# Kernel optimization log

Hardware: AMD Instinct MI355X
Metric: run time of the kernel (lower is better)

## Reference

```python
import jax, jax.numpy as jnp
import numpy as np

N_HEADS = 4
N_HIDDEN = 64  # out_features (concat=False)
MASK_FILL = -9e15
ADJ_THRESH = 0.05


def setup_inputs() -> dict:
    key = jax.random.key(0)
    k1, k2, k3, k4 = jax.random.split(key, 4)
    B, S, N, F = 32, 20, 128, 64
    h = jax.random.normal(k1, (B, S, N, F), dtype=jnp.float32)
    adj_mat = jax.random.uniform(k2, (B, S, N, N), dtype=jnp.float32)
    W = jax.random.normal(k3, (F, N_HEADS * N_HIDDEN), dtype=jnp.float32) * (1.0 / np.sqrt(F))
    a = jax.random.normal(k4, (N_HEADS, 2 * N_HIDDEN, 1), dtype=jnp.float32) * 0.1
    return {"h": h, "adj_mat": adj_mat, "W": W, "a": a}


def reference(h, adj_mat, W, a):
    B, S, N, _ = h.shape
    # Linear projection (no bias); dropout is a no-op (training=False)
    ht = jnp.einsum('bsnf,fo->bsno', h, W)
    # (B, S, H, N, D)
    ht = ht.reshape(B, S, N, N_HEADS, N_HIDDEN).transpose(0, 1, 3, 2, 4)
    a_src = a[:, :N_HIDDEN, 0]   # (H, D)
    a_tgt = a[:, N_HIDDEN:, 0]   # (H, D)
    src = jnp.einsum('bshnd,hd->bshn', ht, a_src)  # (B,S,H,N)
    tgt = jnp.einsum('bshnd,hd->bshn', ht, a_tgt)
    # additive sigmoid score: e_ij = sigmoid(src_i + tgt_j)
    e = jax.nn.sigmoid(src[..., :, None] + tgt[..., None, :])  # (B,S,H,N,N)
    mask = (adj_mat < ADJ_THRESH)[:, :, None, :, :]  # broadcast over heads
    e = jnp.where(mask, MASK_FILL, e)
    attn = jax.nn.softmax(e, axis=-1)
    h_prime = jnp.einsum('bshij,bshjd->bshid', attn, ht)
    # concat=False -> mean over heads
    return h_prime.mean(axis=2)  # (B,S,N,D)
```

## Files before the change

kernel.cpp:

```cpp
#include <hip/hip_runtime.h>
#include <hip/hip_bf16.h>

#define ADJ_TH 0.05f

typedef __bf16 bf16x8 __attribute__((ext_vector_type(8)));
typedef __bf16 bf16x4 __attribute__((ext_vector_type(4)));
typedef float  f32x4  __attribute__((ext_vector_type(4)));

__global__ __launch_bounds__(256)
void prep_kernel(const float* __restrict__ W, const float* __restrict__ a,
                 __bf16* __restrict__ Wt, __bf16* __restrict__ WAt) {
    const int t = threadIdx.x, blk = blockIdx.x;
    if (blk < 64) {
        int id = blk * 256 + t;
        int o = id >> 6, k = id & 63;
        Wt[o * 64 + k] = (__bf16)W[k * 256 + o];
    } else if (blk < 72) {
        int n = blk - 64, hh = n >> 1, st = n & 1;
        int f = t >> 2, p = t & 3;
        const float* wp = W + f * 256 + hh * 64 + p * 16;
        const float* ap = a + hh * 128 + st * 64 + p * 16;
        float s = 0.f;
        #pragma unroll
        for (int d = 0; d < 16; ++d) s += wp[d] * ap[d];
        s += __shfl_xor(s, 1);
        s += __shfl_xor(s, 2);
        if (p == 0) WAt[n * 64 + f] = (__bf16)s;
    } else {
        WAt[512 + t] = (__bf16)0.f;
        WAt[768 + t] = (__bf16)0.f;
    }
}

__device__ __forceinline__ int sw_idx(int o, int i) {
    return o * 128 + ((((i >> 3) ^ o) & 15) << 3) + (i & 7);
}

__global__ __launch_bounds__(256, 3)
void gat_main_kernel(const float* __restrict__ hg, const float* __restrict__ adj,
                     const __bf16* __restrict__ Wt, const __bf16* __restrict__ WAt,
                     float* __restrict__ out)
{
    const int bs  = blockIdx.x;
    const int tid = threadIdx.x;
    const int w   = tid >> 6;
    const int l   = tid & 63;
    const int l15 = l & 15;
    const int l4  = l >> 4;

    __shared__ __bf16   ht_t[128 * 128];
    __shared__ float    src_sh[4][128];
    __shared__ float    tgt_sh[4][128];
    __shared__ unsigned mask_sh[512];

    const float* hb = hg  + (size_t)bs * 8192;
    const float* ab = adj + (size_t)bs * 16384;

    bf16x8 af[2][2];
    #pragma unroll
    for (int m2 = 0; m2 < 2; ++m2) {
        int row = 16 * (2 * w + m2) + l15;
        #pragma unroll
        for (int ks = 0; ks < 2; ++ks) {
            const float4* p4 = reinterpret_cast<const float4*>(hb + row * 64 + 8 * l4 + 32 * ks);
            float4 lo = p4[0], hi = p4[1];
            bf16x8 v;
            v[0]=(__bf16)lo.x; v[1]=(__bf16)lo.y; v[2]=(__bf16)lo.z; v[3]=(__bf16)lo.w;
            v[4]=(__bf16)hi.x; v[5]=(__bf16)hi.y; v[6]=(__bf16)hi.z; v[7]=(__bf16)hi.w;
            af[m2][ks] = v;
        }
    }

    {
        bf16x8 wa0 = *reinterpret_cast<const bf16x8*>(WAt + l15 * 64 + 8 * l4);
        bf16x8 wa1 = *reinterpret_cast<const bf16x8*>(WAt + l15 * 64 + 8 * l4 + 32);
        #pragma unroll
        for (int m2 = 0; m2 < 2; ++m2) {
            f32x4 acc = {0.f,0.f,0.f,0.f};
            acc = __builtin_amdgcn_mfma_f32_16x16x32_bf16(af[m2][0], wa0, acc, 0,0,0);
            acc = __builtin_amdgcn_mfma_f32_16x16x32_bf16(af[m2][1], wa1, acc, 0,0,0);
            if (l15 < 8) {
                int hh = l15 >> 1;
                float* dst = (l15 & 1) ? tgt_sh[hh] : src_sh[hh];
                int i0 = 16 * (2 * w + m2) + 4 * l4;
                #pragma unroll
                for (int r = 0; r < 4; ++r) dst[i0 + r] = acc[r];
            }
        }
    }

    auto gemm1 = [&](int p) {
        #pragma unroll
        for (int nt = 0; nt < 8; ++nt) {
            int oloc = 16 * nt + l15;
            const __bf16* wp = Wt + (size_t)(128 * p + oloc) * 64 + 8 * l4;
            bf16x8 b0 = *reinterpret_cast<const bf16x8*>(wp);
            bf16x8 b1 = *reinterpret_cast<const bf16x8*>(wp + 32);
            #pragma unroll
            for (int m2 = 0; m2 < 2; ++m2) {
                f32x4 acc = {0.f,0.f,0.f,0.f};
                acc = __builtin_amdgcn_mfma_f32_16x16x32_bf16(af[m2][0], b0, acc, 0,0,0);
                acc = __builtin_amdgcn_mfma_f32_16x16x32_bf16(af[m2][1], b1, acc, 0,0,0);
                int i0 = 16 * (2 * w + m2) + 4 * l4;
                bf16x4 st;
                st[0]=(__bf16)acc[0]; st[1]=(__bf16)acc[1];
                st[2]=(__bf16)acc[2]; st[3]=(__bf16)acc[3];
                *reinterpret_cast<bf16x4*>(&ht_t[sw_idx(oloc, i0)]) = st;
            }
        }
    };

    gemm1(0);

    #pragma unroll 4
    for (int rd = 0; rd < 16; ++rd) {
        float4 f = *reinterpret_cast<const float4*>(ab + rd * 1024 + w * 256 + 4 * l);
        unsigned long long b0 = __ballot(f.x < ADJ_TH);
        unsigned long long b1 = __ballot(f.y < ADJ_TH);
        unsigned long long b2 = __ballot(f.z < ADJ_TH);
        unsigned long long b3 = __ballot(f.w < ADJ_TH);
        if (l < 2) {
            int row = 8 * rd + 2 * w + l;
            uint4 v;
            v.x = (unsigned)(b0 >> (32 * l));
            v.y = (unsigned)(b1 >> (32 * l));
            v.z = (unsigned)(b2 >> (32 * l));
            v.w = (unsigned)(b3 >> (32 * l));
            *reinterpret_cast<uint4*>(&mask_sh[row * 4]) = v;
        }
    }

    f32x4 acc2[2][4];
    #pragma unroll
    for (int m2 = 0; m2 < 2; ++m2)
        #pragma unroll
        for (int nt = 0; nt < 4; ++nt) { f32x4 z = {0.f,0.f,0.f,0.f}; acc2[m2][nt] = z; }

    auto phase2 = [&](int p) {
        #pragma unroll 1
        for (int hp = 0; hp < 2; ++hp) {
            int hh = 2 * p + hp;
            float tg[4][8];
            #pragma unroll
            for (int ks = 0; ks < 4; ++ks) {
                const float4* tp = reinterpret_cast<const float4*>(&tgt_sh[hh][8 * l4 + 32 * ks]);
                float4 t0 = tp[0], t1 = tp[1];
                tg[ks][0]=t0.x; tg[ks][1]=t0.y; tg[ks][2]=t0.z; tg[ks][3]=t0.w;
                tg[ks][4]=t1.x; tg[ks][5]=t1.y; tg[ks][6]=t1.z; tg[ks][7]=t1.w;
            }

            bf16x8 pa[2][4];
            #pragma unroll
            for (int m2 = 0; m2 < 2; ++m2) {
                int irow = 16 * (2 * w + m2) + l15;
                float si = src_sh[hh][irow];
                uint4 mm = *reinterpret_cast<const uint4*>(&mask_sh[irow * 4]);
                unsigned mw[4] = {mm.x, mm.y, mm.z, mm.w};
                float pf[4][8];
                float dloc = 0.f;
                #pragma unroll
                for (int ks = 0; ks < 4; ++ks) {
                    #pragma unroll
                    for (int e = 0; e < 8; ++e) {
                        float x  = si + tg[ks][e];
                        float sg = __builtin_amdgcn_rcpf(1.0f + __expf(-x));
                        float pe = __expf(sg);
                        float pv = ((mw[e & 3] >> (8 * ks + 2 * l4 + (e >> 2))) & 1u) ? 0.f : pe;
                        pf[ks][e] = pv;
                        dloc += pv;
                    }
                }
                dloc += __shfl_xor(dloc, 16);
                dloc += __shfl_xor(dloc, 32);
                float scale = 0.25f * __builtin_amdgcn_rcpf(fmaxf(dloc, 1e-20f));
                #pragma unroll
                for (int ks = 0; ks < 4; ++ks) {
                    bf16x8 v;
                    #pragma unroll
                    for (int e = 0; e < 8; ++e) v[e] = (__bf16)(pf[ks][e] * scale);
                    pa[m2][ks] = v;
                }
            }

            #pragma unroll
            for (int nt = 0; nt < 4; ++nt)
                #pragma unroll
                for (int ks = 0; ks < 4; ++ks) {
                    bf16x8 b = *reinterpret_cast<const bf16x8*>(
                        &ht_t[sw_idx(64 * hp + 16 * nt + l15, 8 * l4 + 32 * ks)]);
                    acc2[0][nt] = __builtin_amdgcn_mfma_f32_16x16x32_bf16(pa[0][ks], b, acc2[0][nt], 0,0,0);
                    acc2[1][nt] = __builtin_amdgcn_mfma_f32_16x16x32_bf16(pa[1][ks], b, acc2[1][nt], 0,0,0);
                }
        }
    };

    __syncthreads();
    phase2(0);
    __syncthreads();
    gemm1(1);
    __syncthreads();
    phase2(1);

    float* ob = out + (size_t)bs * 8192;
    #pragma unroll
    for (int m2 = 0; m2 < 2; ++m2)
        #pragma unroll
        for (int nt = 0; nt < 4; ++nt)
            #pragma unroll
            for (int r = 0; r < 4; ++r)
                ob[(32 * w + 16 * m2 + 4 * l4 + r) * 64 + 16 * nt + l15] = acc2[m2][nt][r];
}

extern "C" void kernel_launch(void* const* d_in, const int* in_sizes, int n_in,
                              void* d_out, int out_size, void* d_ws, size_t ws_size,
                              hipStream_t stream) {
    const float* h   = (const float*)d_in[0];
    const float* adj = (const float*)d_in[1];
    const float* W   = (const float*)d_in[2];
    const float* a   = (const float*)d_in[3];
    float* out = (float*)d_out;

    __bf16* Wt  = (__bf16*)d_ws;
    __bf16* WAt = (__bf16*)((char*)d_ws + 32768);

    prep_kernel<<<73, 256, 0, stream>>>(W, a, Wt, WAt);
    gat_main_kernel<<<640, 256, 0, stream>>>(h, adj, Wt, WAt, out);
}
```

Baseline: 138.3 us.

## Use 8 waves per block with one 16-row tile per wave

The main kernel now launches 512 threads per block instead of 256. Each of the 8 waves owns a single 16-row slab instead of two, so the per-wave projection, softmax and attention-matmul work is halved and registers per wave go down. The launch bounds move to (512, 6) to allow more resident waves and more latency hiding on the exp-heavy softmax. In exchange, each wave now reloads the shared weight and ht_t tiles for only half the rows, which doubles LDS read traffic per output row, and __syncthreads now spans more waves.

```diff
diff --git a/kernel.cpp b/kernel.cpp
--- a/kernel.cpp
+++ b/kernel.cpp
@@ -36,7 +36,7 @@
     return o * 128 + ((((i >> 3) ^ o) & 15) << 3) + (i & 7);
 }
 
-__global__ __launch_bounds__(256, 3)
+__global__ __launch_bounds__(512, 6)
 void gat_main_kernel(const float* __restrict__ hg, const float* __restrict__ adj,
                      const __bf16* __restrict__ Wt, const __bf16* __restrict__ WAt,
                      float* __restrict__ out)
@@ -56,10 +56,9 @@
     const float* hb = hg  + (size_t)bs * 8192;
     const float* ab = adj + (size_t)bs * 16384;
 
-    bf16x8 af[2][2];
-    #pragma unroll
-    for (int m2 = 0; m2 < 2; ++m2) {
-        int row = 16 * (2 * w + m2) + l15;
+    bf16x8 af[2];
+    {
+        int row = 16 * w + l15;
         #pragma unroll
         for (int ks = 0; ks < 2; ++ks) {
             const float4* p4 = reinterpret_cast<const float4*>(hb + row * 64 + 8 * l4 + 32 * ks);
@@ -67,25 +66,22 @@
             bf16x8 v;
             v[0]=(__bf16)lo.x; v[1]=(__bf16)lo.y; v[2]=(__bf16)lo.z; v[3]=(__bf16)lo.w;
             v[4]=(__bf16)hi.x; v[5]=(__bf16)hi.y; v[6]=(__bf16)hi.z; v[7]=(__bf16)hi.w;
-            af[m2][ks] = v;
+            af[ks] = v;
         }
     }
 
     {
         bf16x8 wa0 = *reinterpret_cast<const bf16x8*>(WAt + l15 * 64 + 8 * l4);
         bf16x8 wa1 = *reinterpret_cast<const bf16x8*>(WAt + l15 * 64 + 8 * l4 + 32);
-        #pragma unroll
-        for (int m2 = 0; m2 < 2; ++m2) {
-            f32x4 acc = {0.f,0.f,0.f,0.f};
-            acc = __builtin_amdgcn_mfma_f32_16x16x32_bf16(af[m2][0], wa0, acc, 0,0,0);
-            acc = __builtin_amdgcn_mfma_f32_16x16x32_bf16(af[m2][1], wa1, acc, 0,0,0);
-            if (l15 < 8) {
-                int hh = l15 >> 1;
-                float* dst = (l15 & 1) ? tgt_sh[hh] : src_sh[hh];
-                int i0 = 16 * (2 * w + m2) + 4 * l4;
-                #pragma unroll
-                for (int r = 0; r < 4; ++r) dst[i0 + r] = acc[r];
-            }
+        f32x4 acc = {0.f,0.f,0.f,0.f};
+        acc = __builtin_amdgcn_mfma_f32_16x16x32_bf16(af[0], wa0, acc, 0,0,0);
+        acc = __builtin_amdgcn_mfma_f32_16x16x32_bf16(af[1], wa1, acc, 0,0,0);
+        if (l15 < 8) {
+            int hh = l15 >> 1;
+            float* dst = (l15 & 1) ? tgt_sh[hh] : src_sh[hh];
+            int i0 = 16 * w + 4 * l4;
+            #pragma unroll
+            for (int r = 0; r < 4; ++r) dst[i0 + r] = acc[r];
         }
     }
 
@@ -96,31 +92,28 @@
             const __bf16* wp = Wt + (size_t)(128 * p + oloc) * 64 + 8 * l4;
             bf16x8 b0 = *reinterpret_cast<const bf16x8*>(wp);
             bf16x8 b1 = *reinterpret_cast<const bf16x8*>(wp + 32);
-            #pragma unroll
-            for (int m2 = 0; m2 < 2; ++m2) {
-                f32x4 acc = {0.f,0.f,0.f,0.f};
-                acc = __builtin_amdgcn_mfma_f32_16x16x32_bf16(af[m2][0], b0, acc, 0,0,0);
-                acc = __builtin_amdgcn_mfma_f32_16x16x32_bf16(af[m2][1], b1, acc, 0,0,0);
-                int i0 = 16 * (2 * w + m2) + 4 * l4;
-                bf16x4 st;
-                st[0]=(__bf16)acc[0]; st[1]=(__bf16)acc[1];
-                st[2]=(__bf16)acc[2]; st[3]=(__bf16)acc[3];
-                *reinterpret_cast<bf16x4*>(&ht_t[sw_idx(oloc, i0)]) = st;
-            }
+            f32x4 acc = {0.f,0.f,0.f,0.f};
+            acc = __builtin_amdgcn_mfma_f32_16x16x32_bf16(af[0], b0, acc, 0,0,0);
+            acc = __builtin_amdgcn_mfma_f32_16x16x32_bf16(af[1], b1, acc, 0,0,0);
+            int i0 = 16 * w + 4 * l4;
+            bf16x4 st;
+            st[0]=(__bf16)acc[0]; st[1]=(__bf16)acc[1];
+            st[2]=(__bf16)acc[2]; st[3]=(__bf16)acc[3];
+            *reinterpret_cast<bf16x4*>(&ht_t[sw_idx(oloc, i0)]) = st;
         }
     };
 
     gemm1(0);
 
     #pragma unroll 4
-    for (int rd = 0; rd < 16; ++rd) {
-        float4 f = *reinterpret_cast<const float4*>(ab + rd * 1024 + w * 256 + 4 * l);
+    for (int rd = 0; rd < 8; ++rd) {
+        float4 f = *reinterpret_cast<const float4*>(ab + rd * 2048 + w * 256 + 4 * l);
         unsigned long long b0 = __ballot(f.x < ADJ_TH);
         unsigned long long b1 = __ballot(f.y < ADJ_TH);
         unsigned long long b2 = __ballot(f.z < ADJ_TH);
         unsigned long long b3 = __ballot(f.w < ADJ_TH);
         if (l < 2) {
-            int row = 8 * rd + 2 * w + l;
+            int row = 16 * rd + 2 * w + l;
             uint4 v;
             v.x = (unsigned)(b0 >> (32 * l));
             v.y = (unsigned)(b1 >> (32 * l));
@@ -130,11 +123,9 @@
         }
     }
 
-    f32x4 acc2[2][4];
+    f32x4 acc2[4];
     #pragma unroll
-    for (int m2 = 0; m2 < 2; ++m2)
-        #pragma unroll
-        for (int nt = 0; nt < 4; ++nt) { f32x4 z = {0.f,0.f,0.f,0.f}; acc2[m2][nt] = z; }
+    for (int nt = 0; nt < 4; ++nt) { f32x4 z = {0.f,0.f,0.f,0.f}; acc2[nt] = z; }
 
     auto phase2 = [&](int p) {
         #pragma unroll 1
@@ -149,37 +140,34 @@
                 tg[ks][4]=t1.x; tg[ks][5]=t1.y; tg[ks][6]=t1.z; tg[ks][7]=t1.w;
             }
 
-            bf16x8 pa[2][4];
-            #pragma unroll
-            for (int m2 = 0; m2 < 2; ++m2) {
-                int irow = 16 * (2 * w + m2) + l15;
-                float si = src_sh[hh][irow];
-                uint4 mm = *reinterpret_cast<const uint4*>(&mask_sh[irow * 4]);
-                unsigned mw[4] = {mm.x, mm.y, mm.z, mm.w};
-                float pf[4][8];
-                float dloc = 0.f;
+            int irow = 16 * w + l15;
+            float si = src_sh[hh][irow];
+            uint4 mm = *reinterpret_cast<const uint4*>(&mask_sh[irow * 4]);
+            unsigned mw[4] = {mm.x, mm.y, mm.z, mm.w};
+            float pf[4][8];
+            float dloc = 0.f;
+            #pragma unroll
+            for (int ks = 0; ks < 4; ++ks) {
                 #pragma unroll
-                for (int ks = 0; ks < 4; ++ks) {
-                    #pragma unroll
-                    for (int e = 0; e < 8; ++e) {
-                        float x  = si + tg[ks][e];
-                        float sg = __builtin_amdgcn_rcpf(1.0f + __expf(-x));
-                        float pe = __expf(sg);
-                        float pv = ((mw[e & 3] >> (8 * ks + 2 * l4 + (e >> 2))) & 1u) ? 0.f : pe;
-                        pf[ks][e] = pv;
-                        dloc += pv;
-                    }
+                for (int e = 0; e < 8; ++e) {
+                    float x  = si + tg[ks][e];
+                    float sg = __builtin_amdgcn_rcpf(1.0f + __expf(-x));
+                    float pe = __expf(sg);
+                    float pv = ((mw[e & 3] >> (8 * ks + 2 * l4 + (e >> 2))) & 1u) ? 0.f : pe;
+                    pf[ks][e] = pv;
+                    dloc += pv;
                 }
-                dloc += __shfl_xor(dloc, 16);
-                dloc += __shfl_xor(dloc, 32);
-                float scale = 0.25f * __builtin_amdgcn_rcpf(fmaxf(dloc, 1e-20f));
+            }
+            dloc += __shfl_xor(dloc, 16);
+            dloc += __shfl_xor(dloc, 32);
+            float scale = 0.25f * __builtin_amdgcn_rcpf(fmaxf(dloc, 1e-20f));
+            bf16x8 pa[4];
+            #pragma unroll
+            for (int ks = 0; ks < 4; ++ks) {
+                bf16x8 v;
                 #pragma unroll
-                for (int ks = 0; ks < 4; ++ks) {
-                    bf16x8 v;
-                    #pragma unroll
-                    for (int e = 0; e < 8; ++e) v[e] = (__bf16)(pf[ks][e] * scale);
-                    pa[m2][ks] = v;
-                }
+                for (int e = 0; e < 8; ++e) v[e] = (__bf16)(pf[ks][e] * scale);
+                pa[ks] = v;
             }
 
             #pragma unroll
@@ -188,8 +176,7 @@
                 for (int ks = 0; ks < 4; ++ks) {
                     bf16x8 b = *reinterpret_cast<const bf16x8*>(
                         &ht_t[sw_idx(64 * hp + 16 * nt + l15, 8 * l4 + 32 * ks)]);
-                    acc2[0][nt] = __builtin_amdgcn_mfma_f32_16x16x32_bf16(pa[0][ks], b, acc2[0][nt], 0,0,0);
-                    acc2[1][nt] = __builtin_amdgcn_mfma_f32_16x16x32_bf16(pa[1][ks], b, acc2[1][nt], 0,0,0);
+                    acc2[nt] = __builtin_amdgcn_mfma_f32_16x16x32_bf16(pa[ks], b, acc2[nt], 0,0,0);
                 }
         }
     };
@@ -203,12 +190,10 @@
 
     float* ob = out + (size_t)bs * 8192;
     #pragma unroll
-    for (int m2 = 0; m2 < 2; ++m2)
-        #pragma unroll
-        for (int nt = 0; nt < 4; ++nt)
-            #pragma unroll
-            for (int r = 0; r < 4; ++r)
-                ob[(32 * w + 16 * m2 + 4 * l4 + r) * 64 + 16 * nt + l15] = acc2[m2][nt][r];
+    for (int nt = 0; nt < 4; ++nt)
+        #pragma unroll
+        for (int r = 0; r < 4; ++r)
+            ob[(16 * w + 4 * l4 + r) * 64 + 16 * nt + l15] = acc2[nt][r];
 }
 
 extern "C" void kernel_launch(void* const* d_in, const int* in_sizes, int n_in,
@@ -224,5 +209,5 @@
     __bf16* WAt = (__bf16*)((char*)d_ws + 32768);
 
     prep_kernel<<<73, 256, 0, stream>>>(W, a, Wt, WAt);
-    gat_main_kernel<<<640, 256, 0, stream>>>(h, adj, Wt, WAt, out);
-}
+    gat_main_kernel<<<640, 512, 0, stream>>>(h, adj, Wt, WAt, out);
+}
```

Result: slower. 165.9 us (+20.0%).
